# Kernel tuning notes

Measured on AMD Instinct MI355X. Metric: run time of the kernel, lower is better.

## Reference

```python
import jax, jax.numpy as jnp
import numpy as np

N_NODES = 8192
N_EDGES = 524288
D_IN = 256
D_OUT = 256


def setup_inputs() -> dict:
    key = jax.random.key(0)
    ks = jax.random.split(key, 8)
    h = jax.random.normal(ks[0], (N_NODES, D_IN), dtype=jnp.float32)
    # Xavier-uniform-like scale for weights
    s = (6.0 / (D_IN + D_OUT)) ** 0.5
    W = jax.random.uniform(ks[1], (D_IN, D_OUT), jnp.float32, -s, s)
    Wq = jax.random.uniform(ks[2], (D_IN, D_OUT), jnp.float32, -s, s)
    bq = jnp.zeros((D_OUT,), jnp.float32)
    Wk = jax.random.uniform(ks[3], (D_IN, D_OUT), jnp.float32, -s, s)
    bk = jnp.zeros((D_OUT,), jnp.float32)
    senders = jax.random.randint(ks[4], (N_EDGES,), 0, N_NODES, dtype=jnp.int64 if jax.config.jax_enable_x64 else jnp.int32)
    receivers = jax.random.randint(ks[5], (N_EDGES,), 0, N_NODES, dtype=jnp.int64 if jax.config.jax_enable_x64 else jnp.int32)
    return {"h": h, "W": W, "Wq": Wq, "bq": bq, "Wk": Wk, "bk": bk,
            "senders": senders, "receivers": receivers}


def reference(h, W, Wq, bq, Wk, bk, senders, receivers):
    # Projected node features: (N, D_OUT)
    h_proj = jnp.dot(h, W)
    # Dense attention logits a = q @ k^T: (N, N), as in the original module
    q = jnp.dot(h, Wq) + bq
    k = jnp.dot(h, Wk) + bk
    a = jnp.dot(q, k.T)
    # Gather per-edge messages and attention weights, weight, scatter-add
    messages = h_proj[senders] * a[senders, receivers][:, None]  # (E, D_OUT)
    aggregated = jax.ops.segment_sum(messages, receivers, num_segments=h.shape[0])
    return jax.nn.relu(aggregated)
```

## Files before the change

### kernel.cpp

```cpp
#include <hip/hip_runtime.h>
#include <stdint.h>

typedef unsigned short u16;
typedef unsigned int u32;
typedef short v8s __attribute__((ext_vector_type(8)));
typedef float v4f __attribute__((ext_vector_type(4)));

#define N_NODES 8192
#define N_EDGES 524288
#define DFEAT 256
#define PAD 160

static __device__ __forceinline__ float bflo(u32 u) { return __uint_as_float(u << 16); }
static __device__ __forceinline__ float bfhi(u32 u) { return __uint_as_float(u & 0xffff0000u); }
static __device__ __forceinline__ u16 f2bf(float f) {
    u32 u = __float_as_uint(f);
    u32 r = (u + 0x7fffu + ((u >> 16) & 1u)) >> 16;
    return (u16)r;
}

__global__ void prep(const float* __restrict__ h,
                     const float* __restrict__ w0, const float* __restrict__ w1,
                     const float* __restrict__ w2,
                     const int* __restrict__ recv, const int* __restrict__ send,
                     u16* __restrict__ hb, u16* __restrict__ wt,
                     int* __restrict__ cnt, int* __restrict__ es_pad) {
    __shared__ u16 t[64][65];
    int b = blockIdx.x;
    if (b < 2048) {
        int i = (b * 256 + threadIdx.x) * 4;
        float4 v = *(const float4*)(h + i);
        uint2 p;
        p.x = (u32)f2bf(v.x) | ((u32)f2bf(v.y) << 16);
        p.y = (u32)f2bf(v.z) | ((u32)f2bf(v.w) << 16);
        *(uint2*)(hb + i) = p;
    } else if (b < 2096) {
        int bb = b - 2048;
        int region = bb >> 4;
        int tile = bb & 15;
        int k0 = (tile >> 2) * 64, n0 = (tile & 3) * 64;
        const float* w = (region == 0) ? w0 : ((region == 1) ? w1 : w2);
        int tx = threadIdx.x & 63, ty = threadIdx.x >> 6;
#pragma unroll
        for (int it = 0; it < 16; it++) {
            int row = it * 4 + ty;
            t[row][tx] = f2bf(w[(k0 + row) * 256 + n0 + tx]);
        }
        __syncthreads();
        u16* o = wt + region * 65536;
#pragma unroll
        for (int it = 0; it < 16; it++) {
            int row = it * 4 + ty;
            o[(n0 + row) * 256 + k0 + tx] = t[tx][row];
        }
    } else {
        int e = (b - 2096) * 256 + threadIdx.x;
        int r = recv[e];
        int pos = atomicAdd(&cnt[r], 1);
        if (pos < PAD) es_pad[r * PAD + pos] = send[e];
    }
}

__global__ __launch_bounds__(256) void gemm_proj(
    const u16* __restrict__ h, const u16* __restrict__ wt,
    const float* __restrict__ bq, const float* __restrict__ bk,
    u16* __restrict__ hproj, u16* __restrict__ qb, u16* __restrict__ kb) {
    int wave = threadIdx.x >> 6;
    int lane = threadIdx.x & 63;
    int lm = lane & 15;
    int lq = lane >> 4;
    int m0 = blockIdx.x * 64 + wave * 16;
    int region = blockIdx.y >> 2;
    int n0b = (blockIdx.y & 3) * 64;
    const u16* wtr = wt + region * 65536;

    v4f acc[4];
#pragma unroll
    for (int nt = 0; nt < 4; nt++) acc[nt] = (v4f){0.f, 0.f, 0.f, 0.f};

    const u16* arow = h + (m0 + lm) * 256 + lq * 8;
#pragma unroll
    for (int k0 = 0; k0 < 256; k0 += 32) {
        v8s a = *(const v8s*)(arow + k0);
#pragma unroll
        for (int nt = 0; nt < 4; nt++) {
            v8s b = *(const v8s*)(wtr + (n0b + nt * 16 + lm) * 256 + k0 + lq * 8);
            acc[nt] = __builtin_amdgcn_mfma_f32_16x16x32_bf16(a, b, acc[nt], 0, 0, 0);
        }
    }

    u16* outp = (region == 0) ? hproj : ((region == 1) ? qb : kb);
    const float* bias = (region == 1) ? bq : ((region == 2) ? bk : nullptr);
#pragma unroll
    for (int nt = 0; nt < 4; nt++) {
        int n = n0b + nt * 16 + lm;
        float bv = bias ? bias[n] : 0.f;
#pragma unroll
        for (int i = 0; i < 4; i++) {
            int m = m0 + lq * 4 + i;
            outp[m * 256 + n] = f2bf(acc[nt][i] + bv);
        }
    }
}

__global__ __launch_bounds__(256) void edge_fused(
    const u16* __restrict__ qb, const u16* __restrict__ kb, const u16* __restrict__ hpb,
    const int* __restrict__ cnt, const int* __restrict__ es_pad,
    float* __restrict__ out) {
    __shared__ float sc[4][16];
    __shared__ int   ss[4][16];
    int wave = threadIdx.x >> 6;
    int lane = threadIdx.x & 63;
    int r = blockIdx.x * 4 + wave;
    int lm = lane & 15, lq = lane >> 4;
    int lh = lane & 31, half = lane >> 5;
    int colbase = lh * 8;
    int n = min(cnt[r], PAD);
    int base = r * PAD;

    v8s kf[8];
    const u16* krow = kb + r * 256 + lq * 8;
#pragma unroll
    for (int t = 0; t < 8; t++) kf[t] = *(const v8s*)(krow + t * 32);

    float a[8];
#pragma unroll
    for (int i = 0; i < 8; i++) a[i] = 0.f;

    for (int c0 = 0; c0 < n; c0 += 16) {
        int j = c0 + lm;
        if (j >= n) j = n - 1;
        int s = es_pad[base + j];
        const u16* qrow = qb + s * 256 + lq * 8;
        v4f acc = (v4f){0.f, 0.f, 0.f, 0.f};
#pragma unroll
        for (int t = 0; t < 8; t++) {
            v8s av = *(const v8s*)(qrow + t * 32);
            acc = __builtin_amdgcn_mfma_f32_16x16x32_bf16(av, kf[t], acc, 0, 0, 0);
        }
        if (lm == 0) {
#pragma unroll
            for (int i = 0; i < 4; i++) sc[wave][lq * 4 + i] = acc[i];
        }
        if (lq == 0) ss[wave][lm] = s;
        __threadfence_block();

        int m = n - c0;
        if (m >= 16) {
#pragma unroll
            for (int t0 = 0; t0 < 8; t0++) {
                int t = t0 * 2 + half;
                float p = sc[wave][t];
                int s2 = ss[wave][t];
                uint4 hv = *(const uint4*)(hpb + s2 * 256 + colbase);
                a[0] += p * bflo(hv.x); a[1] += p * bfhi(hv.x);
                a[2] += p * bflo(hv.y); a[3] += p * bfhi(hv.y);
                a[4] += p * bflo(hv.z); a[5] += p * bfhi(hv.z);
                a[6] += p * bflo(hv.w); a[7] += p * bfhi(hv.w);
            }
        } else {
            for (int t = half; t < m; t += 2) {
                float p = sc[wave][t];
                int s2 = ss[wave][t];
                uint4 hv = *(const uint4*)(hpb + s2 * 256 + colbase);
                a[0] += p * bflo(hv.x); a[1] += p * bfhi(hv.x);
                a[2] += p * bflo(hv.y); a[3] += p * bfhi(hv.y);
                a[4] += p * bflo(hv.z); a[5] += p * bfhi(hv.z);
                a[6] += p * bflo(hv.w); a[7] += p * bfhi(hv.w);
            }
        }
    }

#pragma unroll
    for (int i = 0; i < 8; i++) a[i] += __shfl_xor(a[i], 32, 64);

    if (half == 0) {
        float4 o0, o1;
        o0.x = fmaxf(a[0], 0.f); o0.y = fmaxf(a[1], 0.f);
        o0.z = fmaxf(a[2], 0.f); o0.w = fmaxf(a[3], 0.f);
        o1.x = fmaxf(a[4], 0.f); o1.y = fmaxf(a[5], 0.f);
        o1.z = fmaxf(a[6], 0.f); o1.w = fmaxf(a[7], 0.f);
        float* op = out + r * 256 + colbase;
        *(float4*)op = o0;
        *(float4*)(op + 4) = o1;
    }
}

extern "C" void kernel_launch(void* const* d_in, const int* in_sizes, int n_in,
                              void* d_out, int out_size, void* d_ws, size_t ws_size,
                              hipStream_t stream) {
    const float* h  = (const float*)d_in[0];
    const float* W  = (const float*)d_in[1];
    const float* Wq = (const float*)d_in[2];
    const float* bq = (const float*)d_in[3];
    const float* Wk = (const float*)d_in[4];
    const float* bk = (const float*)d_in[5];
    const int* senders   = (const int*)d_in[6];
    const int* receivers = (const int*)d_in[7];
    float* out = (float*)d_out;

    char* ws = (char*)d_ws;
    u16* wt     = (u16*)ws;
    u16* hb     = (u16*)(ws + 393216);
    u16* hproj  = hb + N_NODES * DFEAT;
    u16* qb     = hproj + N_NODES * DFEAT;
    u16* kb     = qb + N_NODES * DFEAT;
    int* cnt    = (int*)(kb + N_NODES * DFEAT);
    int* es_pad = cnt + N_NODES;

    hipMemsetAsync(cnt, 0, N_NODES * sizeof(int), stream);
    prep<<<4144, 256, 0, stream>>>(h, W, Wq, Wk, receivers, senders, hb, wt, cnt, es_pad);
    gemm_proj<<<dim3(128, 12), 256, 0, stream>>>(hb, wt, bq, bk, hproj, qb, kb);
    edge_fused<<<N_NODES / 4, 256, 0, stream>>>(qb, kb, hproj, cnt, es_pad, out);
}
```

Measured before the change: 182.2 us.

## Gather q and hproj rows straight into LDS with async global_load_lds

In the edge kernel, each 16-edge chunk's sender q rows and hproj rows are now fetched with global_load_lds directly into a per-wave LDS tile. Both gathers are issued together before one vmcnt wait. Before, the hproj gather could only start after the q·k MFMA finished, so the two loads ran one after the other; issuing them together is meant to raise memory-level parallelism, and the LDS sender-index array is dropped. The cost is 64KB of LDS per block, which limits how many blocks fit on a CU. There is also no double buffering, so each chunk still waits for its whole transfer.

```diff
diff --git a/kernel.cpp b/kernel.cpp
--- a/kernel.cpp
+++ b/kernel.cpp
@@ -10,6 +10,9 @@
 #define N_EDGES 524288
 #define DFEAT 256
 #define PAD 160
+
+typedef __attribute__((address_space(3))) void lds_t;
+typedef const __attribute__((address_space(1))) void gbl_t;
 
 static __device__ __forceinline__ float bflo(u32 u) { return __uint_as_float(u << 16); }
 static __device__ __forceinline__ float bfhi(u32 u) { return __uint_as_float(u & 0xffff0000u); }
@@ -107,16 +110,19 @@
     const u16* __restrict__ qb, const u16* __restrict__ kb, const u16* __restrict__ hpb,
     const int* __restrict__ cnt, const int* __restrict__ es_pad,
     float* __restrict__ out) {
+    __shared__ char lds[65536];
     __shared__ float sc[4][16];
-    __shared__ int   ss[4][16];
     int wave = threadIdx.x >> 6;
     int lane = threadIdx.x & 63;
     int r = blockIdx.x * 4 + wave;
     int lm = lane & 15, lq = lane >> 4;
     int lh = lane & 31, half = lane >> 5;
-    int colbase = lh * 8;
     int n = min(cnt[r], PAD);
     int base = r * PAD;
+    char* qtile = lds + wave * 16384;
+    char* htile = qtile + 8192;
+    const char* qg = (const char*)qb;
+    const char* hg = (const char*)hpb;
 
     v8s kf[8];
     const u16* krow = kb + r * 256 + lq * 8;
@@ -128,31 +134,41 @@
     for (int i = 0; i < 8; i++) a[i] = 0.f;
 
     for (int c0 = 0; c0 < n; c0 += 16) {
-        int j = c0 + lm;
-        if (j >= n) j = n - 1;
-        int s = es_pad[base + j];
-        const u16* qrow = qb + s * 256 + lq * 8;
+        int jq = c0 + lm;
+        if (jq >= n) jq = n - 1;
+        int sq = es_pad[base + jq];
+
+        long qoff = (long)sq * 512 + lq * 16;
+#pragma unroll
+        for (int t = 0; t < 8; t++)
+            __builtin_amdgcn_global_load_lds((gbl_t*)(qg + qoff + t * 64),
+                                             (lds_t*)(qtile + t * 1024), 16, 0, 0);
+#pragma unroll
+        for (int u = 0; u < 8; u++) {
+            int sh = __shfl(sq, 2 * u + half, 64);
+            __builtin_amdgcn_global_load_lds((gbl_t*)(hg + (long)sh * 512 + lh * 16),
+                                             (lds_t*)(htile + u * 1024), 16, 0, 0);
+        }
+        __asm volatile("s_waitcnt vmcnt(0)" ::: "memory");
+
         v4f acc = (v4f){0.f, 0.f, 0.f, 0.f};
 #pragma unroll
         for (int t = 0; t < 8; t++) {
-            v8s av = *(const v8s*)(qrow + t * 32);
+            v8s av = *(const v8s*)(qtile + t * 1024 + lane * 16);
             acc = __builtin_amdgcn_mfma_f32_16x16x32_bf16(av, kf[t], acc, 0, 0, 0);
         }
         if (lm == 0) {
 #pragma unroll
             for (int i = 0; i < 4; i++) sc[wave][lq * 4 + i] = acc[i];
         }
-        if (lq == 0) ss[wave][lm] = s;
         __threadfence_block();
 
         int m = n - c0;
         if (m >= 16) {
 #pragma unroll
             for (int t0 = 0; t0 < 8; t0++) {
-                int t = t0 * 2 + half;
-                float p = sc[wave][t];
-                int s2 = ss[wave][t];
-                uint4 hv = *(const uint4*)(hpb + s2 * 256 + colbase);
+                float p = sc[wave][2 * t0 + half];
+                uint4 hv = *(const uint4*)(htile + t0 * 1024 + half * 512 + lh * 16);
                 a[0] += p * bflo(hv.x); a[1] += p * bfhi(hv.x);
                 a[2] += p * bflo(hv.y); a[3] += p * bfhi(hv.y);
                 a[4] += p * bflo(hv.z); a[5] += p * bfhi(hv.z);
@@ -161,8 +177,7 @@
         } else {
             for (int t = half; t < m; t += 2) {
                 float p = sc[wave][t];
-                int s2 = ss[wave][t];
-                uint4 hv = *(const uint4*)(hpb + s2 * 256 + colbase);
+                uint4 hv = *(const uint4*)(htile + (t >> 1) * 1024 + (t & 1) * 512 + lh * 16);
                 a[0] += p * bflo(hv.x); a[1] += p * bfhi(hv.x);
                 a[2] += p * bflo(hv.y); a[3] += p * bfhi(hv.y);
                 a[4] += p * bflo(hv.z); a[5] += p * bfhi(hv.z);
@@ -180,7 +195,7 @@
         o0.z = fmaxf(a[2], 0.f); o0.w = fmaxf(a[3], 0.f);
         o1.x = fmaxf(a[4], 0.f); o1.y = fmaxf(a[5], 0.f);
         o1.z = fmaxf(a[6], 0.f); o1.w = fmaxf(a[7], 0.f);
-        float* op = out + r * 256 + colbase;
+        float* op = out + r * 256 + lh * 8;
         *(float4*)op = o0;
         *(float4*)(op + 4) = o1;
     }
```

Result: slower. 190.2 us (+4.4%).
